# Kernel optimization log

Hardware: AMD Instinct MI355X
Metric: run time of the kernel (lower is better)

## Reference

```python
import jax, jax.numpy as jnp
import numpy as np

H = 4096      # hidden_size
D = 1024      # mem_dim
A = 512       # attn_dim
B, LQ, TM = 4, 2048, 1500
EPS = 1e-5


def _layernorm(x, w, b):
    mu = jnp.mean(x, axis=-1, keepdims=True)
    var = jnp.var(x, axis=-1, keepdims=True)
    return (x - mu) * jax.lax.rsqrt(var + EPS) * w + b


def setup_inputs() -> dict:
    key = jax.random.key(0)
    ks = jax.random.split(key, 12)
    s = lambda fan_in: 1.0 / np.sqrt(fan_in)
    return {
        "hidden": jax.random.normal(ks[0], (B, LQ, H), jnp.float32),
        "mem": jax.random.normal(ks[1], (B, TM, D), jnp.float32),
        "mem_mask": jnp.zeros((B, TM), dtype=bool),
        "Wq": jax.random.uniform(ks[2], (H, A), jnp.float32, -s(H), s(H)),
        "bq": jnp.zeros((A,), jnp.float32),
        "Wk": jax.random.uniform(ks[3], (D, A), jnp.float32, -s(D), s(D)),
        "bk": jnp.zeros((A,), jnp.float32),
        "Wv": jax.random.uniform(ks[4], (D, A), jnp.float32, -s(D), s(D)),
        "bv": jnp.zeros((A,), jnp.float32),
        "Wo": jax.random.uniform(ks[5], (A, H), jnp.float32, -s(A), s(A)),
        "bo": jnp.zeros((H,), jnp.float32),
        "ln_in_w": jnp.ones((H,), jnp.float32),
        "ln_in_b": jnp.zeros((H,), jnp.float32),
        "ln_out_w": jnp.ones((H,), jnp.float32),
        "ln_out_b": jnp.zeros((H,), jnp.float32),
        "gate_logit": jnp.float32(-2.0),
    }


def reference(hidden, mem, mem_mask, Wq, bq, Wk, bk, Wv, bv, Wo, bo,
              ln_in_w, ln_in_b, ln_out_w, ln_out_b, gate_logit):
    h_norm = _layernorm(hidden, ln_in_w, ln_in_b)            # [B,LQ,H]
    Q = h_norm @ Wq + bq                                     # [B,LQ,A]
    K = mem @ Wk + bk                                        # [B,TM,A]
    V = mem @ Wv + bv                                        # [B,TM,A]
    scale = 1.0 / jnp.sqrt(jnp.float32(Q.shape[-1]))
    scores = jnp.einsum('bqa,bka->bqk', Q, K) * scale        # [B,LQ,TM]
    scores = jnp.where(mem_mask[:, None, :], jnp.float32(-1e30), scores)
    attn = jax.nn.softmax(scores, axis=-1)
    context = jnp.einsum('bqk,bka->bqa', attn, V)            # [B,LQ,A]
    context_h = context @ Wo + bo                            # [B,LQ,H]
    out_base = _layernorm(hidden + context_h, ln_out_w, ln_out_b)
    g = jax.nn.sigmoid(gate_logit)
    return hidden + g * (out_base - hidden)
```

## Files before the change

### kernel.cpp

```cpp
#include <hip/hip_runtime.h>
#include <cstdint>
#include <cstddef>

#define H_   4096
#define D_   1024
#define A_   512
#define B_   4
#define LQ_  2048
#define TM_  1500
#define TMP_ 1536
#define EPS_ 1e-5f

typedef __attribute__((ext_vector_type(8))) _Float16 half8;
typedef __attribute__((ext_vector_type(4))) _Float16 half4v;
typedef __attribute__((ext_vector_type(4))) float f32x4;

__device__ __forceinline__ void gload_lds16(void* g, void* l) {
  __builtin_amdgcn_global_load_lds((__attribute__((address_space(1))) void*)g,
                                   (__attribute__((address_space(3))) void*)l,
                                   16, 0, 0);
}

template <int OUTMODE>
__device__ __forceinline__ void gemm_tile(
    const _Float16* __restrict__ A, int lda,
    const _Float16* __restrict__ Bt, int ldb,
    const float* __restrict__ bias,
    void* __restrict__ C, int ldc,
    int Mvalid, int m0, int n0, int kbase, int kiters, float scale,
    _Float16* As, _Float16* Bs,
    const unsigned char* __restrict__ mrow, float* __restrict__ lsum, int nvalid) {
  const int tid = threadIdx.x;
  const int lane = tid & 63;
  const int wave = tid >> 6;

  f32x4 acc[4][4];
#pragma unroll
  for (int i = 0; i < 4; ++i)
#pragma unroll
    for (int jj = 0; jj < 4; ++jj) acc[i][jj] = (f32x4){0.f, 0.f, 0.f, 0.f};

  const _Float16* gA[2];
  const _Float16* gB[2];
  _Float16* lA[2];
  _Float16* lB[2];
#pragma unroll
  for (int i = 0; i < 2; ++i) {
    const int c = wave * 64 + lane + 256 * i;
    const int r = c >> 2;
    const int cs = c & 3;
    const int col = (cs ^ ((r >> 1) & 3)) * 8;
    int ra = m0 + r;
    if (ra >= Mvalid) ra = Mvalid - 1;
    gA[i] = A + (size_t)ra * lda + kbase + col;
    gB[i] = Bt + (size_t)(n0 + r) * ldb + kbase + col;
    lA[i] = As + wave * 512 + i * 2048;
    lB[i] = Bs + wave * 512 + i * 2048;
  }

  const int wm = (wave >> 1) * 64;
  const int wn = (wave & 1) * 64;
  const int rsub = lane & 15;
  const int j = lane >> 4;
  const int slot = j ^ ((rsub >> 1) & 3);

  for (int kt = 0; kt < kiters; ++kt) {
    const int ko = kt * 32;
#pragma unroll
    for (int i = 0; i < 2; ++i) {
      gload_lds16((void*)(gA[i] + ko), (void*)lA[i]);
      gload_lds16((void*)(gB[i] + ko), (void*)lB[i]);
    }
    __syncthreads();
    half8 af[4], bfr[4];
#pragma unroll
    for (int x = 0; x < 4; ++x) {
      af[x]  = *(const half8*)&As[(wm + x * 16 + rsub) * 32 + slot * 8];
      bfr[x] = *(const half8*)&Bs[(wn + x * 16 + rsub) * 32 + slot * 8];
    }
#pragma unroll
    for (int mi = 0; mi < 4; ++mi)
#pragma unroll
      for (int ni = 0; ni < 4; ++ni)
        acc[mi][ni] = __builtin_amdgcn_mfma_f32_16x16x32_f16(af[mi], bfr[ni], acc[mi][ni], 0, 0, 0);
    __syncthreads();
  }

  const int cn = n0 + wn + rsub;
  const int rm = m0 + wm + j * 4;

  if (OUTMODE == 3) {
    bool ok[4];
#pragma unroll
    for (int ni = 0; ni < 4; ++ni) {
      const int n = cn + ni * 16;
      const int nc = n < nvalid ? n : nvalid - 1;
      ok[ni] = (n < nvalid) && (mrow[nc] == 0);
    }
#pragma unroll
    for (int mi = 0; mi < 4; ++mi) {
#pragma unroll
      for (int r = 0; r < 4; ++r) {
        const int m = rm + mi * 16 + r;
        float rowsum = 0.f;
#pragma unroll
        for (int ni = 0; ni < 4; ++ni) {
          const int n = cn + ni * 16;
          const float e = ok[ni] ? __expf(acc[mi][ni][r] * scale) : 0.f;
          ((_Float16*)C)[(size_t)m * ldc + n] = (_Float16)e;
          rowsum += e;
        }
#pragma unroll
        for (int d = 1; d < 16; d <<= 1) rowsum += __shfl_xor(rowsum, d);
        if (rsub == 0) atomicAdd(&lsum[m], rowsum);
      }
    }
    return;
  }

  if (OUTMODE == 1) {
#pragma unroll
    for (int ni = 0; ni < 4; ++ni) {
      const int n = cn + ni * 16;
      const float bi = bias ? bias[n] : 0.f;
#pragma unroll
      for (int mi = 0; mi < 4; ++mi) {
        half4v pk;
#pragma unroll
        for (int r = 0; r < 4; ++r) pk[r] = (_Float16)(acc[mi][ni][r] * scale + bi);
        *(half4v*)&((_Float16*)C)[(size_t)n * ldc + rm + mi * 16] = pk;
      }
    }
    return;
  }

#pragma unroll
  for (int ni = 0; ni < 4; ++ni) {
    const int n = cn + ni * 16;
    const float bi = (OUTMODE == 0 && bias) ? bias[n] : 0.f;
#pragma unroll
    for (int mi = 0; mi < 4; ++mi) {
#pragma unroll
      for (int r = 0; r < 4; ++r) {
        const int m = rm + mi * 16 + r;
        const float v = acc[mi][ni][r] * scale + bi;
        if (OUTMODE == 0) ((_Float16*)C)[(size_t)m * ldc + n] = (_Float16)v;
        else ((float*)C)[(size_t)m * ldc + n] = v;
      }
    }
  }
}

template <int OUTMODE>
__global__ __launch_bounds__(256) void gemm_nt_kernel(
    const _Float16* __restrict__ Aall, size_t strideA, int lda,
    const _Float16* __restrict__ Btall, size_t strideB, int ldb,
    const float* __restrict__ bias,
    void* __restrict__ Call, size_t strideC, size_t strideS,
    int ldc, int Mvalid, int kiters, int nslices, int sliceK, float scale) {
  __shared__ __align__(16) _Float16 As[4096];
  __shared__ __align__(16) _Float16 Bs[4096];
  const int nx = gridDim.x, ny = gridDim.y;
  int id = (int)blockIdx.x + nx * ((int)blockIdx.y + ny * (int)blockIdx.z);
  const int tot = nx * ny * (int)gridDim.z;
  id = (id & 7) * (tot >> 3) + (id >> 3);
  const int bx = id % nx;
  const int by = (id / nx) % ny;
  const int bz = id / (nx * ny);
  const int batch = bz / nslices;
  const int slice = bz % nslices;
  const _Float16* A = Aall + (size_t)batch * strideA;
  const _Float16* Bt = Btall + (size_t)batch * strideB;
  char* C = (char*)Call + ((size_t)batch * strideC + (size_t)slice * strideS) *
                          (OUTMODE == 2 ? 4 : 2);
  gemm_tile<OUTMODE>(A, lda, Bt, ldb, bias, (void*)C, ldc, Mvalid,
                     by * 128, bx * 128, slice * sliceK, kiters,
                     scale, As, Bs, nullptr, nullptr, 0);
}

__global__ __launch_bounds__(256) void scores_kernel(
    const _Float16* __restrict__ Qh, const _Float16* __restrict__ Kp,
    _Float16* __restrict__ sc, const unsigned char* __restrict__ mask,
    float* __restrict__ lsum) {
  __shared__ __align__(16) _Float16 As[4096];
  __shared__ __align__(16) _Float16 Bs[4096];
  const int nx = gridDim.x, ny = gridDim.y;
  int id = (int)blockIdx.x + nx * ((int)blockIdx.y + ny * (int)blockIdx.z);
  const int tot = nx * ny * (int)gridDim.z;
  id = (id & 7) * (tot >> 3) + (id >> 3);
  const int bx = id % nx;
  const int by = (id / nx) % ny;
  const int b = id / (nx * ny);
  gemm_tile<3>(Qh + (size_t)b * LQ_ * A_, A_, Kp + (size_t)b * TMP_ * A_, A_, nullptr,
               (void*)(sc + (size_t)b * LQ_ * TMP_), TMP_, LQ_,
               by * 128, bx * 128, 0, 16, 0.044194173824159216f,
               As, Bs, mask + (size_t)b * TM_, lsum + (size_t)b * LQ_, TM_);
}

__global__ __launch_bounds__(256) void qkv_kernel(
    const _Float16* __restrict__ hnorm, const _Float16* __restrict__ WqT,
    float* __restrict__ Qpart,
    const _Float16* __restrict__ memh, const _Float16* __restrict__ WkT,
    const float* __restrict__ bk, _Float16* __restrict__ Kp,
    const _Float16* __restrict__ WvT, const float* __restrict__ bv,
    _Float16* __restrict__ VT) {
  __shared__ __align__(16) _Float16 As[4096];
  __shared__ __align__(16) _Float16 Bs[4096];
  const int bid0 = blockIdx.x;
  if (bid0 < 512) {
    const int bid = ((bid0 & 7) << 6) | (bid0 >> 3);
    const int nb = bid & 3, mb = (bid >> 2) & 63, ks = bid >> 8;
    gemm_tile<2>(hnorm, H_, WqT, H_, nullptr,
                 (void*)(Qpart + (size_t)ks * 8192 * A_), A_,
                 8192, mb * 128, nb * 128, ks * 2048, 64, 1.f, As, Bs,
                 nullptr, nullptr, 0);
  } else if (bid0 < 704) {
    int t = bid0 - 512;
    t = (t & 7) * 24 + (t >> 3);
    const int nb = t & 3, mb = (t >> 2) % 12, b = t / 48;
    gemm_tile<0>(memh + (size_t)b * TM_ * D_, D_, WkT, D_, bk,
                 (void*)(Kp + (size_t)b * TMP_ * A_), A_,
                 TM_, mb * 128, nb * 128, 0, 32, 1.f, As, Bs,
                 nullptr, nullptr, 0);
  } else {
    int t = bid0 - 704;
    t = (t & 7) * 24 + (t >> 3);
    const int nb = t & 3, mb = (t >> 2) % 12, b = t / 48;
    gemm_tile<1>(memh + (size_t)b * TM_ * D_, D_, WvT, D_, bv,
                 (void*)(VT + (size_t)b * A_ * TMP_), TMP_,
                 TM_, mb * 128, nb * 128, 0, 32, 1.f, As, Bs,
                 nullptr, nullptr, 0);
  }
}

__global__ __launch_bounds__(256) void qreduce_kernel(
    const float* __restrict__ p, const float* __restrict__ bias,
    _Float16* __restrict__ out, float* __restrict__ lsum) {
  const int bid = blockIdx.x;
  if (bid >= 4096) {
    lsum[(bid - 4096) * 256 + threadIdx.x] = 0.f;
    return;
  }
  const size_t i = ((size_t)bid * 256 + threadIdx.x) * 4;
  const float4 a = *(const float4*)(p + i);
  const float4 b = *(const float4*)(p + (size_t)8192 * A_ + i);
  const float4 bi = *(const float4*)(bias + (i & (A_ - 1)));
  half4v o;
  o.x = (_Float16)(a.x + b.x + bi.x);
  o.y = (_Float16)(a.y + b.y + bi.y);
  o.z = (_Float16)(a.z + b.z + bi.z);
  o.w = (_Float16)(a.w + b.w + bi.w);
  *(half4v*)(out + i) = o;
}

__global__ __launch_bounds__(256) void areduce_kernel(
    const float* __restrict__ p, const float* __restrict__ lsum,
    _Float16* __restrict__ out) {
  const size_t S = (size_t)B_ * LQ_ * A_;
  const size_t i = ((size_t)blockIdx.x * 256 + threadIdx.x) * 4;
  const float4 a = *(const float4*)(p + i);
  const float4 b = *(const float4*)(p + S + i);
  const float4 c = *(const float4*)(p + 2 * S + i);
  const float inv = 1.f / lsum[i >> 9];
  half4v o;
  o.x = (_Float16)((a.x + b.x + c.x) * inv);
  o.y = (_Float16)((a.y + b.y + c.y) * inv);
  o.z = (_Float16)((a.z + b.z + c.z) * inv);
  o.w = (_Float16)((a.w + b.w + c.w) * inv);
  *(half4v*)(out + i) = o;
}

__global__ __launch_bounds__(256) void ln1_kernel(
    const float* __restrict__ hidden, const float* __restrict__ lnw,
    const float* __restrict__ lnb, _Float16* __restrict__ hnorm) {
  const int t = threadIdx.x;
  const int lane = t & 63;
  const int row = blockIdx.x * 4 + (t >> 6);
  const float* x = hidden + (size_t)row * H_;
  _Float16* y = hnorm + (size_t)row * H_;
  float4 v[16];
  float s = 0.f, ss = 0.f;
#pragma unroll
  for (int i = 0; i < 16; ++i) {
    v[i] = ((const float4*)x)[lane + 64 * i];
    s  += v[i].x + v[i].y + v[i].z + v[i].w;
    ss += v[i].x * v[i].x + v[i].y * v[i].y + v[i].z * v[i].z + v[i].w * v[i].w;
  }
#pragma unroll
  for (int off = 32; off; off >>= 1) { s += __shfl_xor(s, off); ss += __shfl_xor(ss, off); }
  const float mu = s * (1.f / H_);
  const float var = ss * (1.f / H_) - mu * mu;
  const float rstd = rsqrtf(var + EPS_);
#pragma unroll
  for (int i = 0; i < 16; ++i) {
    float4 wv4 = ((const float4*)lnw)[lane + 64 * i];
    float4 bv4 = ((const float4*)lnb)[lane + 64 * i];
    half4v o;
    o.x = (_Float16)((v[i].x - mu) * rstd * wv4.x + bv4.x);
    o.y = (_Float16)((v[i].y - mu) * rstd * wv4.y + bv4.y);
    o.z = (_Float16)((v[i].z - mu) * rstd * wv4.z + bv4.z);
    o.w = (_Float16)((v[i].w - mu) * rstd * wv4.w + bv4.w);
    ((half4v*)y)[lane + 64 * i] = o;
  }
}

__global__ __launch_bounds__(256) void misc_kernel(
    const float* __restrict__ mem, _Float16* __restrict__ memh,
    const float* __restrict__ Wq, _Float16* __restrict__ WqT,
    const float* __restrict__ Wk, _Float16* __restrict__ WkT,
    const float* __restrict__ Wv, _Float16* __restrict__ WvT,
    const float* __restrict__ Wo, _Float16* __restrict__ WoT) {
  __shared__ float smem[32 * 33];
  int bid = blockIdx.x;
  const int t = threadIdx.x;
  if (bid < 1500) {
    const size_t i = ((size_t)bid * 256 + t) * 4;
    float4 f = *(const float4*)(mem + i);
    half4v o;
    o.x = (_Float16)f.x; o.y = (_Float16)f.y; o.z = (_Float16)f.z; o.w = (_Float16)f.w;
    *(half4v*)(memh + i) = o;
    return;
  }
  bid -= 1500;
  const float* src;
  _Float16* dst;
  int R, C;
  if (bid < 2048) { src = Wq; dst = WqT; R = 4096; C = 512; }
  else if (bid < 2048 + 512) { bid -= 2048; src = Wk; dst = WkT; R = 1024; C = 512; }
  else if (bid < 2048 + 1024) { bid -= 2048 + 512; src = Wv; dst = WvT; R = 1024; C = 512; }
  else { bid -= 2048 + 1024; src = Wo; dst = WoT; R = 512; C = 4096; }
  const int nbx = C / 32;
  const int bx = bid % nbx, by = bid / nbx;
  const int tx = t & 31, ty = t >> 5;
  const int c0 = bx * 32, r0 = by * 32;
#pragma unroll
  for (int i = 0; i < 32; i += 8)
    smem[(ty + i) * 33 + tx] = src[(size_t)(r0 + ty + i) * C + c0 + tx];
  __syncthreads();
  {
    const int q = t & 7, cc = t >> 3;
    half4v g;
#pragma unroll
    for (int e = 0; e < 4; ++e) g[e] = (_Float16)smem[(4 * q + e) * 33 + cc];
    *(half4v*)&dst[(size_t)(c0 + cc) * R + r0 + 4 * q] = g;
  }
}

__global__ __launch_bounds__(256) void ln2_gate_kernel(
    const float* __restrict__ hidden_, const _Float16* __restrict__ ctxh_,
    const float* __restrict__ w, const float* __restrict__ bvec,
    const float* __restrict__ gate_logit, float* __restrict__ out_) {
  const int row = blockIdx.x;
  const float* h = hidden_ + (size_t)row * H_;
  const _Float16* c = ctxh_ + (size_t)row * H_;
  float* o = out_ + (size_t)row * H_;
  const int t = threadIdx.x;
  float4 hv[4];
  float xv[16];
  float s = 0.f, ss = 0.f;
#pragma unroll
  for (int i = 0; i < 4; ++i) {
    hv[i] = ((const float4*)h)[t + 256 * i];
    half4v cv = ((const half4v*)c)[t + 256 * i];
    xv[4 * i + 0] = hv[i].x + (float)cv.x;
    xv[4 * i + 1] = hv[i].y + (float)cv.y;
    xv[4 * i + 2] = hv[i].z + (float)cv.z;
    xv[4 * i + 3] = hv[i].w + (float)cv.w;
    s  += xv[4 * i + 0] + xv[4 * i + 1] + xv[4 * i + 2] + xv[4 * i + 3];
    ss += xv[4 * i + 0] * xv[4 * i + 0] + xv[4 * i + 1] * xv[4 * i + 1] +
          xv[4 * i + 2] * xv[4 * i + 2] + xv[4 * i + 3] * xv[4 * i + 3];
  }
  __shared__ float red[2][4];
  const int lane = t & 63, wv = t >> 6;
#pragma unroll
  for (int off = 32; off; off >>= 1) { s += __shfl_down(s, off); ss += __shfl_down(ss, off); }
  if (lane == 0) { red[0][wv] = s; red[1][wv] = ss; }
  __syncthreads();
  s  = red[0][0] + red[0][1] + red[0][2] + red[0][3];
  ss = red[1][0] + red[1][1] + red[1][2] + red[1][3];
  const float mu = s * (1.f / H_);
  const float var = ss * (1.f / H_) - mu * mu;
  const float rstd = rsqrtf(var + EPS_);
  const float g = 1.f / (1.f + __expf(-gate_logit[0]));
#pragma unroll
  for (int i = 0; i < 4; ++i) {
    float4 wv4 = ((const float4*)w)[t + 256 * i];
    float4 bv4 = ((const float4*)bvec)[t + 256 * i];
    float4 ov;
    ov.x = hv[i].x + g * ((xv[4 * i + 0] - mu) * rstd * wv4.x + bv4.x - hv[i].x);
    ov.y = hv[i].y + g * ((xv[4 * i + 1] - mu) * rstd * wv4.y + bv4.y - hv[i].y);
    ov.z = hv[i].z + g * ((xv[4 * i + 2] - mu) * rstd * wv4.z + bv4.z - hv[i].z);
    ov.w = hv[i].w + g * ((xv[4 * i + 3] - mu) * rstd * wv4.w + bv4.w - hv[i].w);
    ((float4*)o)[t + 256 * i] = ov;
  }
}

extern "C" void kernel_launch(void* const* d_in, const int* in_sizes, int n_in,
                              void* d_out, int out_size, void* d_ws, size_t ws_size,
                              hipStream_t stream) {
  const float* hidden = (const float*)d_in[0];
  const float* mem    = (const float*)d_in[1];
  const unsigned char* mask = (const unsigned char*)d_in[2];
  const float* Wq = (const float*)d_in[3];
  const float* bq = (const float*)d_in[4];
  const float* Wk = (const float*)d_in[5];
  const float* bk = (const float*)d_in[6];
  const float* Wv = (const float*)d_in[7];
  const float* bv = (const float*)d_in[8];
  const float* Wo = (const float*)d_in[9];
  const float* bo = (const float*)d_in[10];
  const float* lnw1 = (const float*)d_in[11];
  const float* lnb1 = (const float*)d_in[12];
  const float* lnw2 = (const float*)d_in[13];
  const float* lnb2 = (const float*)d_in[14];
  const float* gate = (const float*)d_in[15];
  float* out = (float*)d_out;

  _Float16* p = (_Float16*)d_ws;
  _Float16* hnorm = p; p += (size_t)8192 * H_;
  _Float16* Qh    = p; p += (size_t)8192 * A_;
  _Float16* memh  = p; p += (size_t)6000 * D_;
  _Float16* WqT   = p; p += (size_t)A_ * H_;
  _Float16* WkT   = p; p += (size_t)A_ * D_;
  _Float16* WvT   = p; p += (size_t)A_ * D_;
  _Float16* WoT   = p; p += (size_t)H_ * A_;
  _Float16* Kp    = p; p += (size_t)B_ * TMP_ * A_;
  _Float16* VT    = p; p += (size_t)B_ * A_ * TMP_;
  _Float16* sc    = p; p += (size_t)B_ * LQ_ * TMP_;
  _Float16* ctx   = p; p += (size_t)8192 * A_;
  float* Qpart = (float*)sc;
  float* Apart = (float*)hnorm;
  float* lsum  = (float*)WkT;

  ln1_kernel<<<2048, 256, 0, stream>>>(hidden, lnw1, lnb1, hnorm);
  misc_kernel<<<1500 + 2048 + 512 + 512 + 2048, 256, 0, stream>>>(
      mem, memh, Wq, WqT, Wk, WkT, Wv, WvT, Wo, WoT);
  qkv_kernel<<<896, 256, 0, stream>>>(hnorm, WqT, Qpart, memh, WkT, bk, Kp, WvT, bv, VT);
  qreduce_kernel<<<4096 + 32, 256, 0, stream>>>(Qpart, bq, Qh, lsum);
  scores_kernel<<<dim3(12, 16, 4), 256, 0, stream>>>(Qh, Kp, sc, mask, lsum);
  gemm_nt_kernel<2><<<dim3(4, 16, 12), 256, 0, stream>>>(
      sc, (size_t)LQ_ * TMP_, TMP_, VT, (size_t)A_ * TMP_, TMP_, nullptr,
      (void*)Apart, (size_t)LQ_ * A_, (size_t)B_ * LQ_ * A_, A_, LQ_, 16, 3, 512, 1.f);
  areduce_kernel<<<4096, 256, 0, stream>>>(Apart, lsum, ctx);
  gemm_nt_kernel<0><<<dim3(32, 64, 1), 256, 0, stream>>>(
      ctx, 0, A_, WoT, 0, A_, bo, (void*)hnorm, 0, 0, H_, 8192, 16, 1, 0, 1.f);
  ln2_gate_kernel<<<8192, 256, 0, stream>>>(hidden, hnorm, lnw2, lnb2, gate, out);
}
```

Before: 522.2 us.

## Replace output projection GEMM with 256x256-tile 8-wave pipelined kernel

Swaps the generic 128x128 NT GEMM for the context@Wo projection with a dedicated kernel that uses 256x256 tiles, 512 threads, 128 KB of LDS with a 4-stage ring buffer, and direct global-to-LDS loads issued two K-steps ahead. Wave priority raising around MFMA blocks and split A-fragment loads overlap memory traffic with compute. The larger tile raises arithmetic intensity and cuts redundant operand loads. In exchange occupancy drops to one block per CU, the grid shrinks to 512 blocks, and the fp16 output is written with scattered scalar stores.

```diff
diff --git a/kernel.cpp b/kernel.cpp
--- a/kernel.cpp
+++ b/kernel.cpp
@@ -176,6 +176,129 @@
   gemm_tile<OUTMODE>(A, lda, Bt, ldb, bias, (void*)C, ldc, Mvalid,
                      by * 128, bx * 128, slice * sliceK, kiters,
                      scale, As, Bs, nullptr, nullptr, 0);
+}
+
+#define WO_NKH 16
+__global__ __launch_bounds__(512, 1) void wo8_kernel(
+    const _Float16* __restrict__ Ag,
+    const _Float16* __restrict__ Bg,
+    const float* __restrict__ bias,
+    _Float16* __restrict__ Cg) {
+  __shared__ __align__(16) _Float16 lds[65536];
+  const int tid = threadIdx.x;
+  const int lane = tid & 63;
+  const int wave = tid >> 6;
+  const int wr = wave >> 2;
+  const int wc = wave & 3;
+  int id = (int)blockIdx.x;
+  id = (id & 7) * 64 + (id >> 3);
+  const int by = id >> 4;
+  const int bx = id & 15;
+  const int m0 = by * 256, n0 = bx * 256;
+
+  const _Float16* srcA[2];
+  const _Float16* srcB[2];
+  _Float16* dstA[2];
+  _Float16* dstB[2];
+#pragma unroll
+  for (int p = 0; p < 2; ++p) {
+    const int c = p * 512 + tid;
+    const int r = c >> 2, cs = c & 3;
+    const int col = (cs ^ ((r >> 1) & 3)) * 8;
+    srcA[p] = Ag + (size_t)(m0 + r) * 512 + col;
+    srcB[p] = Bg + (size_t)(n0 + r) * 512 + col;
+    dstA[p] = lds + (p * 512 + wave * 64) * 8;
+    dstB[p] = lds + 32768 + (p * 512 + wave * 64) * 8;
+  }
+
+  const int rsub = lane & 15;
+  const int j = lane >> 4;
+  const int sc_ = j ^ ((rsub >> 1) & 3);
+
+  f32x4 acc[8][4];
+#pragma unroll
+  for (int i = 0; i < 8; ++i)
+#pragma unroll
+    for (int n = 0; n < 4; ++n) acc[i][n] = (f32x4){0.f, 0.f, 0.f, 0.f};
+
+#pragma unroll
+  for (int p = 0; p < 2; ++p) gload_lds16((void*)(srcA[p]), (void*)(dstA[p]));
+#pragma unroll
+  for (int p = 0; p < 2; ++p) gload_lds16((void*)(srcB[p]), (void*)(dstB[p]));
+#pragma unroll
+  for (int p = 0; p < 2; ++p) gload_lds16((void*)(srcA[p] + 32), (void*)(dstA[p] + 8192));
+#pragma unroll
+  for (int p = 0; p < 2; ++p) gload_lds16((void*)(srcB[p] + 32), (void*)(dstB[p] + 8192));
+  asm volatile("s_waitcnt vmcnt(4)" ::: "memory");
+  __builtin_amdgcn_s_barrier();
+
+  half8 bf[4];
+  for (int h = 0; h < WO_NKH; ++h) {
+    const int sl = h & 3;
+    const _Float16* Asl = lds + sl * 8192;
+    const _Float16* Bsl = lds + 32768 + sl * 8192;
+    if (h + 2 < WO_NKH) {
+      const int s2 = (h + 2) & 3;
+#pragma unroll
+      for (int p = 0; p < 2; ++p)
+        gload_lds16((void*)(srcA[p] + (h + 2) * 32), (void*)(dstA[p] + s2 * 8192));
+    }
+    half8 af[4];
+#pragma unroll
+    for (int x = 0; x < 4; ++x) {
+      af[x] = *(const half8*)&Asl[(wr * 128 + x * 16 + rsub) * 32 + sc_ * 8];
+      bf[x] = *(const half8*)&Bsl[(wc * 64 + x * 16 + rsub) * 32 + sc_ * 8];
+    }
+    __builtin_amdgcn_s_barrier();
+    __builtin_amdgcn_s_setprio(1);
+#pragma unroll
+    for (int mi = 0; mi < 4; ++mi)
+#pragma unroll
+      for (int ni = 0; ni < 4; ++ni)
+        acc[mi][ni] = __builtin_amdgcn_mfma_f32_16x16x32_f16(af[mi], bf[ni], acc[mi][ni], 0, 0, 0);
+    __builtin_amdgcn_s_setprio(0);
+    __builtin_amdgcn_s_barrier();
+    if (h + 2 < WO_NKH) {
+      const int s2 = (h + 2) & 3;
+#pragma unroll
+      for (int p = 0; p < 2; ++p)
+        gload_lds16((void*)(srcB[p] + (h + 2) * 32), (void*)(dstB[p] + s2 * 8192));
+    }
+#pragma unroll
+    for (int x = 0; x < 4; ++x)
+      af[x] = *(const half8*)&Asl[(wr * 128 + 64 + x * 16 + rsub) * 32 + sc_ * 8];
+    if (h < WO_NKH - 2) {
+      asm volatile("s_waitcnt vmcnt(4)" ::: "memory");
+    } else if (h == WO_NKH - 2) {
+      asm volatile("s_waitcnt vmcnt(0)" ::: "memory");
+    }
+    __builtin_amdgcn_s_barrier();
+    __builtin_amdgcn_s_setprio(1);
+#pragma unroll
+    for (int mi = 0; mi < 4; ++mi)
+#pragma unroll
+      for (int ni = 0; ni < 4; ++ni)
+        acc[4 + mi][ni] = __builtin_amdgcn_mfma_f32_16x16x32_f16(af[mi], bf[ni], acc[4 + mi][ni], 0, 0, 0);
+    __builtin_amdgcn_s_setprio(0);
+    __builtin_amdgcn_s_barrier();
+  }
+
+  const int cn0 = n0 + wc * 64 + rsub;
+  const int rm0 = m0 + wr * 128 + j * 4;
+#pragma unroll
+  for (int ni = 0; ni < 4; ++ni) {
+    const int n = cn0 + ni * 16;
+    const float bi = bias[n];
+#pragma unroll
+    for (int mh = 0; mh < 2; ++mh)
+#pragma unroll
+      for (int mi = 0; mi < 4; ++mi)
+#pragma unroll
+        for (int r = 0; r < 4; ++r) {
+          const int m = rm0 + mh * 64 + mi * 16 + r;
+          Cg[(size_t)m * 4096 + n] = (_Float16)(acc[mh * 4 + mi][ni][r] + bi);
+        }
+  }
 }
 
 __global__ __launch_bounds__(256) void scores_kernel(
@@ -442,7 +565,6 @@
       sc, (size_t)LQ_ * TMP_, TMP_, VT, (size_t)A_ * TMP_, TMP_, nullptr,
       (void*)Apart, (size_t)LQ_ * A_, (size_t)B_ * LQ_ * A_, A_, LQ_, 16, 3, 512, 1.f);
   areduce_kernel<<<4096, 256, 0, stream>>>(Apart, lsum, ctx);
-  gemm_nt_kernel<0><<<dim3(32, 64, 1), 256, 0, stream>>>(
-      ctx, 0, A_, WoT, 0, A_, bo, (void*)hnorm, 0, 0, H_, 8192, 16, 1, 0, 1.f);
+  wo8_kernel<<<512, 512, 0, stream>>>(ctx, WoT, bo, hnorm);
   ln2_gate_kernel<<<8192, 256, 0, stream>>>(hidden, hnorm, lnw2, lnb2, gate, out);
 }
```

Measured after the change: 511.4 us. -2.1%, faster.
